# Kernel optimization log

Hardware: AMD Instinct MI355X
Metric: run time of the kernel (lower is better)

The kernel has to match this reference:

```python
import jax, jax.numpy as jnp
import numpy as np

N_NODES = 100000
N_FEAT = 500
N_HID = 16
N_CLS = 7
N_EDGES = 3200000


def setup_inputs() -> dict:
    key = jax.random.key(0)
    k1, k2, k3, k4 = jax.random.split(key, 4)
    x = jax.random.normal(k1, (N_NODES, N_FEAT), dtype=jnp.float32)
    edge_index = jax.random.randint(k2, (2, N_EDGES), 0, N_NODES, dtype=jnp.int32)
    # Glorot-style init for the two GCNConv weight matrices
    W1 = jax.random.normal(k3, (N_FEAT, N_HID), dtype=jnp.float32) * (1.0 / np.sqrt(N_FEAT))
    b1 = jnp.zeros((N_HID,), dtype=jnp.float32)
    W2 = jax.random.normal(k4, (N_HID, N_CLS), dtype=jnp.float32) * (1.0 / np.sqrt(N_HID))
    b2 = jnp.zeros((N_CLS,), dtype=jnp.float32)
    return {"x": x, "edge_index": edge_index, "W1": W1, "b1": b1, "W2": W2, "b2": b2}


def _gcn_norm(edge_index, n_nodes):
    # Add self-loops, compute symmetric normalization D^-1/2 (A+I) D^-1/2
    loop = jnp.arange(n_nodes, dtype=edge_index.dtype)
    src = jnp.concatenate([edge_index[0], loop])  # [E+N]
    dst = jnp.concatenate([edge_index[1], loop])  # [E+N]
    deg = jax.ops.segment_sum(jnp.ones_like(dst, dtype=jnp.float32), dst, num_segments=n_nodes)
    dinv = jnp.where(deg > 0, jax.lax.rsqrt(deg), 0.0)
    norm = dinv[src] * dinv[dst]  # [E+N]
    return src, dst, norm


def _gcn_conv(h, W, b, src, dst, norm, n_nodes):
    m = h @ W                                   # [N, out] dense projection first (small out dim)
    agg = jax.ops.segment_sum(m[src] * norm[:, None], dst, num_segments=n_nodes)
    return agg + b


def reference(x, edge_index, W1, b1, W2, b2):
    n = x.shape[0]
    src, dst, norm = _gcn_norm(edge_index, n)
    h = jax.nn.relu(_gcn_conv(x, W1, b1, src, dst, norm, n))
    # dropout is identity in eval mode (training=False)
    logits = _gcn_conv(h, W2, b2, src, dst, norm, n)
    return jax.nn.log_softmax(logits, axis=1)
```

## Files before the change

kernel.cpp:

```cpp
#include <hip/hip_runtime.h>
#include <math.h>

#define N_NODES 100000
#define N_EDGES 3200000
#define N_FEAT  500
#define N_HID   16
#define N_CLS   7

#define BKT_SHIFT 7
#define BKT_SIZE  128
#define NBKT      782
#define NBLK_BIN  256
#define EDGES_PER_BLK 12500
#define COUNTS_LEN (NBKT * NBLK_BIN)
#define NBLK_SCANA NBKT
#define SBUF_CAP  5632

#define OFF_DINV   0
#define OFF_COUNTS 100000
#define OFF_BSUM   300192
#define OFF_ROWP   301216
#define OFF_BINNED 401220
#define OFF_SORTED 3601220
#define OFF_WP     6801220
#define OFF_M1S    6809412
#define OFF_M2S    7609412

typedef __attribute__((ext_vector_type(8))) short short8v;
typedef __attribute__((ext_vector_type(4))) float f32x4v;

__device__ inline unsigned short f2bf(float f) {
    unsigned int u = __float_as_uint(f);
    return (unsigned short)((u + 0x7FFF + ((u >> 16) & 1)) >> 16);
}
__device__ inline float bf2f(unsigned short h) {
    return __uint_as_float((unsigned int)h << 16);
}

__global__ __launch_bounds__(1024) void hist(const int* __restrict__ dst,
                                             int* __restrict__ counts) {
    __shared__ int cnt[4][NBKT];
    int t = threadIdx.x, b = blockIdx.x;
    int wq = (t >> 6) & 3;
    for (int i = t; i < 4 * NBKT; i += 1024) ((int*)cnt)[i] = 0;
    __syncthreads();
    const int4* d4 = (const int4*)(dst + b * EDGES_PER_BLK);
    for (int k = t; k < EDGES_PER_BLK / 4; k += 1024) {
        int4 d = d4[k];
        atomicAdd(&cnt[wq][d.x >> BKT_SHIFT], 1);
        atomicAdd(&cnt[wq][d.y >> BKT_SHIFT], 1);
        atomicAdd(&cnt[wq][d.z >> BKT_SHIFT], 1);
        atomicAdd(&cnt[wq][d.w >> BKT_SHIFT], 1);
    }
    __syncthreads();
    for (int i = t; i < NBKT; i += 1024)
        counts[b * NBKT + i] = cnt[0][i] + cnt[1][i] + cnt[2][i] + cnt[3][i];
}

__global__ void scanA(int* __restrict__ counts, int* __restrict__ bsum) {
    __shared__ int s[256];
    int t = threadIdx.x, k = blockIdx.x;
    int v = counts[t * NBKT + k];
    s[t] = v;
    __syncthreads();
    for (int off = 1; off < 256; off <<= 1) {
        int a = (t >= off) ? s[t - off] : 0;
        __syncthreads();
        s[t] += a;
        __syncthreads();
    }
    counts[t * NBKT + k] = s[t] - v;
    if (t == 255) bsum[k] = s[255];
}

__global__ void scanB_wpack(int* __restrict__ bsum, const float* __restrict__ W1,
                            uint4* __restrict__ wp) {
    int t = threadIdx.x;
    {
        int p = t;
        int s = p >> 6, l = p & 63;
        int col = l & 15, kb = s * 32 + (l >> 4) * 8;
        unsigned int hw[4], lw[4];
#pragma unroll
        for (int d = 0; d < 4; ++d) {
            unsigned int hpair = 0, lpair = 0;
#pragma unroll
            for (int e = 0; e < 2; ++e) {
                int k = kb + d * 2 + e;
                float w0 = (k < N_FEAT) ? W1[k * 16 + col] : 0.f;
                unsigned int u = __float_as_uint(w0);
                unsigned int uh = u & 0xFFFF0000u;
                float res = w0 - __uint_as_float(uh);
                hpair |= (uh >> 16) << (16 * e);
                lpair |= (unsigned int)f2bf(res) << (16 * e);
            }
            hw[d] = hpair; lw[d] = lpair;
        }
        wp[p] = make_uint4(hw[0], hw[1], hw[2], hw[3]);
        wp[1024 + p] = make_uint4(lw[0], lw[1], lw[2], lw[3]);
    }
    __shared__ int s[1024];
    int v = (t < NBKT) ? bsum[t] : 0;
    s[t] = v;
    __syncthreads();
    for (int off = 1; off < 1024; off <<= 1) {
        int a = (t >= off) ? s[t - off] : 0;
        __syncthreads();
        s[t] += a;
        __syncthreads();
    }
    if (t < NBKT) bsum[t] = s[t] - v;
}

__global__ __launch_bounds__(1024) void binpass(const int* __restrict__ src,
                        const int* __restrict__ dst,
                        const int* __restrict__ counts, const int* __restrict__ bsum,
                        unsigned int* __restrict__ binned) {
    __shared__ int cur[NBKT];
    int t = threadIdx.x, b = blockIdx.x;
    for (int i = t; i < NBKT; i += 1024) cur[i] = counts[b * NBKT + i] + bsum[i];
    __syncthreads();
    const int4* s4 = (const int4*)(src + b * EDGES_PER_BLK);
    const int4* d4 = (const int4*)(dst + b * EDGES_PER_BLK);
    for (int k = t; k < EDGES_PER_BLK / 4; k += 1024) {
        int4 d = d4[k];
        int4 s = s4[k];
        int pos;
        pos = atomicAdd(&cur[d.x >> BKT_SHIFT], 1);
        binned[pos] = (unsigned int)s.x | ((unsigned int)(d.x & (BKT_SIZE - 1)) << 17);
        pos = atomicAdd(&cur[d.y >> BKT_SHIFT], 1);
        binned[pos] = (unsigned int)s.y | ((unsigned int)(d.y & (BKT_SIZE - 1)) << 17);
        pos = atomicAdd(&cur[d.z >> BKT_SHIFT], 1);
        binned[pos] = (unsigned int)s.z | ((unsigned int)(d.z & (BKT_SIZE - 1)) << 17);
        pos = atomicAdd(&cur[d.w >> BKT_SHIFT], 1);
        binned[pos] = (unsigned int)s.w | ((unsigned int)(d.w & (BKT_SIZE - 1)) << 17);
    }
}

__global__ __launch_bounds__(512) void sortA(const unsigned int* __restrict__ binned,
        const int* __restrict__ bsum,
        int* __restrict__ rowptr, float* __restrict__ dinv) {
    __shared__ int cnt[BKT_SIZE];
    __shared__ int sc[BKT_SIZE];
    int t = threadIdx.x, b = blockIdx.x;
    int beg = bsum[b];
    int end = (b < NBKT - 1) ? bsum[b + 1] : N_EDGES;
    if (t < BKT_SIZE) cnt[t] = 0;
    __syncthreads();
    for (int e = beg + t; e < end; e += 512)
        atomicAdd(&cnt[(binned[e] >> 17) & (BKT_SIZE - 1)], 1);
    __syncthreads();
    int v = (t < BKT_SIZE) ? cnt[t] : 0;
    if (t < BKT_SIZE) sc[t] = v;
    __syncthreads();
    for (int off = 1; off < BKT_SIZE; off <<= 1) {
        int a = (t < BKT_SIZE && t >= off) ? sc[t - off] : 0;
        __syncthreads();
        if (t < BKT_SIZE) sc[t] += a;
        __syncthreads();
    }
    if (t < BKT_SIZE) {
        int g = b * BKT_SIZE + t;
        if (g < N_NODES) {
            rowptr[g] = beg + sc[t] - v;
            dinv[g] = rsqrtf((float)v + 1.0f);
        }
    }
    if (b == 0 && t == 0) rowptr[N_NODES] = N_EDGES;
}

#define G1_NBLK 1563

__device__ inline void split8(const float4 a, const float4 b, short8v& hi, short8v& lo) {
    float f[8] = {a.x, a.y, a.z, a.w, b.x, b.y, b.z, b.w};
#pragma unroll
    for (int i = 0; i < 8; ++i) {
        unsigned int u = __float_as_uint(f[i]);
        unsigned int uh = u & 0xFFFF0000u;
        hi[i] = (short)(u >> 16);
        lo[i] = (short)f2bf(f[i] - __uint_as_float(uh));
    }
}

__global__ __launch_bounds__(256) void gemm1(const float* __restrict__ x,
        const uint4* __restrict__ wp, const float* __restrict__ dinv,
        unsigned short* __restrict__ m1s) {
    __shared__ uint4 swp[2048];
    const int t = threadIdx.x, b = blockIdx.x;
    const int lane = t & 63, w = t >> 6;
#pragma unroll
    for (int i = 0; i < 8; ++i) swp[i * 256 + t] = wp[i * 256 + t];
    __syncthreads();

    const int r16 = lane & 15, g = lane >> 4;
    const int rowbase = b * 64 + w * 16;
    const int row = rowbase + r16;
    const int srow = (row < N_NODES) ? row : 0;
    const float* pA = x + (size_t)srow * N_FEAT + g * 8;
    const float* t0 = (g <= 2) ? pA + 480 : x;
    const float* t1 = (g <= 1) ? pA + 484 : x;

    float4 a0_0 = *(const float4*)(pA);        float4 a1_0 = *(const float4*)(pA + 4);
    float4 a0_1 = *(const float4*)(pA + 32);   float4 a1_1 = *(const float4*)(pA + 36);
    float4 a0_2 = *(const float4*)(pA + 64);   float4 a1_2 = *(const float4*)(pA + 68);
    float4 a0_3 = *(const float4*)(pA + 96);   float4 a1_3 = *(const float4*)(pA + 100);
    float4 a0_4 = *(const float4*)(pA + 128);  float4 a1_4 = *(const float4*)(pA + 132);
    float4 a0_5 = *(const float4*)(pA + 160);  float4 a1_5 = *(const float4*)(pA + 164);

    f32x4v acc = {0.f, 0.f, 0.f, 0.f};
#pragma unroll
    for (int s = 0; s < 16; ++s) {
        float4 xa, xb;
        switch (s % 6) {
            case 0: xa = a0_0; xb = a1_0; break;
            case 1: xa = a0_1; xb = a1_1; break;
            case 2: xa = a0_2; xb = a1_2; break;
            case 3: xa = a0_3; xb = a1_3; break;
            case 4: xa = a0_4; xb = a1_4; break;
            default: xa = a0_5; xb = a1_5; break;
        }
        if (s <= 9) {
            int tg = s + 6;
            const float* p = (tg == 15) ? t0 : pA + tg * 32;
            const float* q = (tg == 15) ? t1 : pA + tg * 32 + 4;
            float4 n0 = *(const float4*)p;
            float4 n1 = *(const float4*)q;
            switch (s % 6) {
                case 0: a0_0 = n0; a1_0 = n1; break;
                case 1: a0_1 = n0; a1_1 = n1; break;
                case 2: a0_2 = n0; a1_2 = n1; break;
                case 3: a0_3 = n0; a1_3 = n1; break;
                case 4: a0_4 = n0; a1_4 = n1; break;
                default: a0_5 = n0; a1_5 = n1; break;
            }
        }
        short8v ah, al;
        split8(xa, xb, ah, al);
        short8v bh = *reinterpret_cast<const short8v*>(&swp[s * 64 + lane]);
        short8v bl = *reinterpret_cast<const short8v*>(&swp[1024 + s * 64 + lane]);
        acc = __builtin_amdgcn_mfma_f32_16x16x32_bf16(ah, bh, acc, 0, 0, 0);
        acc = __builtin_amdgcn_mfma_f32_16x16x32_bf16(al, bh, acc, 0, 0, 0);
        acc = __builtin_amdgcn_mfma_f32_16x16x32_bf16(ah, bl, acc, 0, 0, 0);
    }

#pragma unroll
    for (int j = 0; j < 4; ++j) {
        int r = rowbase + g * 4 + j;
        if (r < N_NODES) m1s[(size_t)r * 16 + r16] = f2bf(acc[j] * dinv[r]);
    }
}

__global__ __launch_bounds__(512) void sortAgg1(const unsigned int* __restrict__ binned,
        const int* __restrict__ bsum,
        const int* __restrict__ rowptr, const float* __restrict__ dinv,
        const unsigned short* __restrict__ m1s, const float* __restrict__ b1,
        const float* __restrict__ W2, unsigned int* __restrict__ sorted,
        unsigned short* __restrict__ m2s) {
    __shared__ unsigned int sbuf[SBUF_CAP];
    __shared__ int cur[BKT_SIZE];
    __shared__ float acc[BKT_SIZE * 17];
    __shared__ float sW2[N_HID * N_CLS];
    __shared__ float sb1[N_HID];
    int t = threadIdx.x, b = blockIdx.x;
    if (t < N_HID * N_CLS) sW2[t] = W2[t];
    if (t < N_HID) sb1[t] = b1[t];
    int beg = bsum[b];
    int end = (b < NBKT - 1) ? bsum[b + 1] : N_EDGES;
    if (t < BKT_SIZE) {
        int g = b * BKT_SIZE + t;
        cur[t] = ((g < N_NODES) ? rowptr[g] : end) - beg;
    }
    __syncthreads();
    for (int e = beg + t; e < end; e += 512) {
        unsigned int u = binned[e];
        int pos = atomicAdd(&cur[(u >> 17) & (BKT_SIZE - 1)], 1);
        if (pos < SBUF_CAP) sbuf[pos] = u & 0x1FFFF;
    }
    __syncthreads();
    int n = end - beg;
    for (int i = t; i < n; i += 512) sorted[beg + i] = sbuf[i];
    {
        int nn = t >> 2, q = t & 3;
        int g = b * BKT_SIZE + nn;
        float a0 = 0.f, a1 = 0.f, a2 = 0.f, a3 = 0.f;
        if (g < N_NODES) {
            int lbeg = rowptr[g] - beg;
            int lend = ((g + 1 <= N_NODES) ? rowptr[g + 1] : N_EDGES) - beg;
            int p = lbeg;
            for (; p + 3 < lend; p += 4) {
                unsigned int s0 = sbuf[p], s1 = sbuf[p + 1];
                unsigned int s2 = sbuf[p + 2], s3 = sbuf[p + 3];
                uint2 w0 = *(const uint2*)&m1s[(size_t)s0 * 16 + q * 4];
                uint2 w1 = *(const uint2*)&m1s[(size_t)s1 * 16 + q * 4];
                uint2 w2 = *(const uint2*)&m1s[(size_t)s2 * 16 + q * 4];
                uint2 w3 = *(const uint2*)&m1s[(size_t)s3 * 16 + q * 4];
                a0 += __uint_as_float(w0.x << 16);
                a1 += __uint_as_float(w0.x & 0xFFFF0000u);
                a2 += __uint_as_float(w0.y << 16);
                a3 += __uint_as_float(w0.y & 0xFFFF0000u);
                a0 += __uint_as_float(w1.x << 16);
                a1 += __uint_as_float(w1.x & 0xFFFF0000u);
                a2 += __uint_as_float(w1.y << 16);
                a3 += __uint_as_float(w1.y & 0xFFFF0000u);
                a0 += __uint_as_float(w2.x << 16);
                a1 += __uint_as_float(w2.x & 0xFFFF0000u);
                a2 += __uint_as_float(w2.y << 16);
                a3 += __uint_as_float(w2.y & 0xFFFF0000u);
                a0 += __uint_as_float(w3.x << 16);
                a1 += __uint_as_float(w3.x & 0xFFFF0000u);
                a2 += __uint_as_float(w3.y << 16);
                a3 += __uint_as_float(w3.y & 0xFFFF0000u);
            }
            for (; p < lend; ++p) {
                unsigned int s0 = sbuf[p];
                uint2 w0 = *(const uint2*)&m1s[(size_t)s0 * 16 + q * 4];
                a0 += __uint_as_float(w0.x << 16);
                a1 += __uint_as_float(w0.x & 0xFFFF0000u);
                a2 += __uint_as_float(w0.y << 16);
                a3 += __uint_as_float(w0.y & 0xFFFF0000u);
            }
        }
        __syncthreads();
        float* ap = &acc[nn * 17 + q * 4];
        ap[0] = a0; ap[1] = a1; ap[2] = a2; ap[3] = a3;
    }
    __syncthreads();
    for (int idx = t; idx < BKT_SIZE * 16; idx += 512) {
        int nn = idx >> 4, jj = idx & 15;
        int gg = b * BKT_SIZE + nn;
        if (gg < N_NODES) {
            float di = dinv[gg];
            float hv = di * (acc[nn * 17 + jj] + bf2f(m1s[(size_t)gg * 16 + jj])) + sb1[jj];
            acc[nn * 17 + jj] = hv > 0.f ? hv : 0.f;
        }
    }
    __syncthreads();
    for (int idx = t; idx < BKT_SIZE * 8; idx += 512) {
        int nn = idx >> 3, cc = idx & 7;
        int gg = b * BKT_SIZE + nn;
        if (gg < N_NODES) {
            float sum = 0.f;
            if (cc < N_CLS) {
#pragma unroll
                for (int jj = 0; jj < N_HID; ++jj) sum += acc[nn * 17 + jj] * sW2[jj * 7 + cc];
                sum *= dinv[gg];
            }
            m2s[(size_t)gg * 8 + cc] = f2bf(sum);
        }
    }
}

__global__ __launch_bounds__(512) void agg2(const unsigned int* __restrict__ sorted,
        const int* __restrict__ rowptr, const float* __restrict__ dinv,
        const unsigned short* __restrict__ m2s, const float* __restrict__ b2,
        float* __restrict__ out) {
    __shared__ float acc[BKT_SIZE * 9];
    int t = threadIdx.x, b = blockIdx.x;
    int n = t >> 2, q = t & 3;
    int g = b * BKT_SIZE + n;
    float a0 = 0.f, a1 = 0.f;
    if (g < N_NODES) {
        int beg = rowptr[g], end = rowptr[g + 1];
        int p = beg;
        for (; (p & 3) && p < end; ++p) {
            unsigned int s0 = sorted[p];
            unsigned int w0 = *(const unsigned int*)&m2s[(size_t)s0 * 8 + q * 2];
            a0 += __uint_as_float(w0 << 16); a1 += __uint_as_float(w0 & 0xFFFF0000u);
        }
        for (; p + 3 < end; p += 4) {
            uint4 sv = *(const uint4*)&sorted[p];
            unsigned int w0 = *(const unsigned int*)&m2s[(size_t)sv.x * 8 + q * 2];
            unsigned int w1 = *(const unsigned int*)&m2s[(size_t)sv.y * 8 + q * 2];
            unsigned int w2 = *(const unsigned int*)&m2s[(size_t)sv.z * 8 + q * 2];
            unsigned int w3 = *(const unsigned int*)&m2s[(size_t)sv.w * 8 + q * 2];
            a0 += __uint_as_float(w0 << 16); a1 += __uint_as_float(w0 & 0xFFFF0000u);
            a0 += __uint_as_float(w1 << 16); a1 += __uint_as_float(w1 & 0xFFFF0000u);
            a0 += __uint_as_float(w2 << 16); a1 += __uint_as_float(w2 & 0xFFFF0000u);
            a0 += __uint_as_float(w3 << 16); a1 += __uint_as_float(w3 & 0xFFFF0000u);
        }
        for (; p < end; ++p) {
            unsigned int s0 = sorted[p];
            unsigned int w0 = *(const unsigned int*)&m2s[(size_t)s0 * 8 + q * 2];
            a0 += __uint_as_float(w0 << 16); a1 += __uint_as_float(w0 & 0xFFFF0000u);
        }
    }
    float* ap = &acc[n * 9 + q * 2];
    ap[0] = a0; ap[1] = a1;
    __syncthreads();
    int j = t & 7;
    for (int pass = 0; pass < 2; ++pass) {
        int nn = (t >> 3) + pass * 64;
        int gg = b * BKT_SIZE + nn;
        bool valid = (gg < N_NODES) && (j < N_CLS);
        float v = -1e30f;
        if (valid) {
            float di = dinv[gg];
            v = di * (acc[nn * 9 + j] + bf2f(m2s[(size_t)gg * 8 + j])) + b2[j];
        }
        float mx = v;
#pragma unroll
        for (int off = 1; off < 8; off <<= 1) mx = fmaxf(mx, __shfl_xor(mx, off, 8));
        float ex = valid ? expf(v - mx) : 0.f;
        float sum = ex;
#pragma unroll
        for (int off = 1; off < 8; off <<= 1) sum += __shfl_xor(sum, off, 8);
        float ls = mx + logf(sum);
        if (valid) out[(size_t)gg * 7 + j] = v - ls;
    }
}

extern "C" void kernel_launch(void* const* d_in, const int* in_sizes, int n_in,
                              void* d_out, int out_size, void* d_ws, size_t ws_size,
                              hipStream_t stream) {
    const float* x  = (const float*)d_in[0];
    const int*   ei = (const int*)d_in[1];
    const float* W1 = (const float*)d_in[2];
    const float* b1 = (const float*)d_in[3];
    const float* W2 = (const float*)d_in[4];
    const float* b2 = (const float*)d_in[5];
    float* out = (float*)d_out;
    char*  wsb = (char*)d_ws;

    const int* src = ei;
    const int* dst = ei + N_EDGES;

    float*          dinv   = (float*)wsb + OFF_DINV;
    int*            counts = (int*)wsb + OFF_COUNTS;
    int*            bsum   = (int*)wsb + OFF_BSUM;
    int*            rowptr = (int*)wsb + OFF_ROWP;
    unsigned int*   binned = (unsigned int*)wsb + OFF_BINNED;
    unsigned int*   sorted = (unsigned int*)wsb + OFF_SORTED;
    uint4*          wp     = (uint4*)((int*)wsb + OFF_WP);
    unsigned short* m1s    = (unsigned short*)(wsb + (size_t)OFF_M1S * 4);
    unsigned short* m2s    = (unsigned short*)(wsb + (size_t)OFF_M2S * 4);

    hist       <<<NBLK_BIN, 1024, 0, stream>>>(dst, counts);
    scanA      <<<NBLK_SCANA, 256, 0, stream>>>(counts, bsum);
    scanB_wpack<<<1, 1024, 0, stream>>>(bsum, W1, wp);
    binpass    <<<NBLK_BIN, 1024, 0, stream>>>(src, dst, counts, bsum, binned);
    sortA      <<<NBKT, 512, 0, stream>>>(binned, bsum, rowptr, dinv);
    gemm1      <<<G1_NBLK, 256, 0, stream>>>(x, wp, dinv, m1s);
    sortAgg1   <<<NBKT, 512, 0, stream>>>(binned, bsum, rowptr, dinv,
                                          m1s, b1, W2, sorted, m2s);
    agg2       <<<NBKT, 512, 0, stream>>>(sorted, rowptr, dinv, m2s, b2, out);
}
```

Before: 418.2 us.

## Split per-node edge gathers across two thread halves with 1024-thread blocks

Doubles block size for sortAgg1 and agg2 so each node's neighbor list is processed by 8 threads, two interleaved halves each summing every other edge. Partial sums go to separate LDS buffers and are combined in the epilogue. This raises memory-level parallelism in the latency-bound gathers. The cost is more LDS per block and the loss of the vectorized uint4 index loads in agg2.

```diff
diff --git a/kernel.cpp b/kernel.cpp
--- a/kernel.cpp
+++ b/kernel.cpp
@@ -250,7 +250,7 @@
     }
 }
 
-__global__ __launch_bounds__(512) void sortAgg1(const unsigned int* __restrict__ binned,
+__global__ __launch_bounds__(1024) void sortAgg1(const unsigned int* __restrict__ binned,
         const int* __restrict__ bsum,
         const int* __restrict__ rowptr, const float* __restrict__ dinv,
         const unsigned short* __restrict__ m1s, const float* __restrict__ b1,
@@ -258,7 +258,7 @@
         unsigned short* __restrict__ m2s) {
     __shared__ unsigned int sbuf[SBUF_CAP];
     __shared__ int cur[BKT_SIZE];
-    __shared__ float acc[BKT_SIZE * 17];
+    __shared__ float acc[2][BKT_SIZE * 17];
     __shared__ float sW2[N_HID * N_CLS];
     __shared__ float sb1[N_HID];
     int t = threadIdx.x, b = blockIdx.x;
@@ -271,25 +271,26 @@
         cur[t] = ((g < N_NODES) ? rowptr[g] : end) - beg;
     }
     __syncthreads();
-    for (int e = beg + t; e < end; e += 512) {
+    for (int e = beg + t; e < end; e += 1024) {
         unsigned int u = binned[e];
         int pos = atomicAdd(&cur[(u >> 17) & (BKT_SIZE - 1)], 1);
         if (pos < SBUF_CAP) sbuf[pos] = u & 0x1FFFF;
     }
     __syncthreads();
     int n = end - beg;
-    for (int i = t; i < n; i += 512) sorted[beg + i] = sbuf[i];
+    for (int i = t; i < n; i += 1024) sorted[beg + i] = sbuf[i];
     {
-        int nn = t >> 2, q = t & 3;
+        int nn = t >> 3, q8 = t & 7;
+        int half = q8 >> 2, q = q8 & 3;
         int g = b * BKT_SIZE + nn;
         float a0 = 0.f, a1 = 0.f, a2 = 0.f, a3 = 0.f;
         if (g < N_NODES) {
             int lbeg = rowptr[g] - beg;
-            int lend = ((g + 1 <= N_NODES) ? rowptr[g + 1] : N_EDGES) - beg;
-            int p = lbeg;
-            for (; p + 3 < lend; p += 4) {
-                unsigned int s0 = sbuf[p], s1 = sbuf[p + 1];
-                unsigned int s2 = sbuf[p + 2], s3 = sbuf[p + 3];
+            int lend = rowptr[g + 1] - beg;
+            int p = lbeg + half;
+            for (; p + 6 < lend; p += 8) {
+                unsigned int s0 = sbuf[p],     s1 = sbuf[p + 2];
+                unsigned int s2 = sbuf[p + 4], s3 = sbuf[p + 6];
                 uint2 w0 = *(const uint2*)&m1s[(size_t)s0 * 16 + q * 4];
                 uint2 w1 = *(const uint2*)&m1s[(size_t)s1 * 16 + q * 4];
                 uint2 w2 = *(const uint2*)&m1s[(size_t)s2 * 16 + q * 4];
@@ -311,7 +312,7 @@
                 a2 += __uint_as_float(w3.y << 16);
                 a3 += __uint_as_float(w3.y & 0xFFFF0000u);
             }
-            for (; p < lend; ++p) {
+            for (; p < lend; p += 2) {
                 unsigned int s0 = sbuf[p];
                 uint2 w0 = *(const uint2*)&m1s[(size_t)s0 * 16 + q * 4];
                 a0 += __uint_as_float(w0.x << 16);
@@ -320,29 +321,29 @@
                 a3 += __uint_as_float(w0.y & 0xFFFF0000u);
             }
         }
-        __syncthreads();
-        float* ap = &acc[nn * 17 + q * 4];
+        float* ap = &acc[half][nn * 17 + q * 4];
         ap[0] = a0; ap[1] = a1; ap[2] = a2; ap[3] = a3;
     }
     __syncthreads();
-    for (int idx = t; idx < BKT_SIZE * 16; idx += 512) {
+    for (int idx = t; idx < BKT_SIZE * 16; idx += 1024) {
         int nn = idx >> 4, jj = idx & 15;
         int gg = b * BKT_SIZE + nn;
         if (gg < N_NODES) {
             float di = dinv[gg];
-            float hv = di * (acc[nn * 17 + jj] + bf2f(m1s[(size_t)gg * 16 + jj])) + sb1[jj];
-            acc[nn * 17 + jj] = hv > 0.f ? hv : 0.f;
-        }
-    }
-    __syncthreads();
-    for (int idx = t; idx < BKT_SIZE * 8; idx += 512) {
+            float hv = di * (acc[0][nn * 17 + jj] + acc[1][nn * 17 + jj]
+                             + bf2f(m1s[(size_t)gg * 16 + jj])) + sb1[jj];
+            acc[0][nn * 17 + jj] = hv > 0.f ? hv : 0.f;
+        }
+    }
+    __syncthreads();
+    for (int idx = t; idx < BKT_SIZE * 8; idx += 1024) {
         int nn = idx >> 3, cc = idx & 7;
         int gg = b * BKT_SIZE + nn;
         if (gg < N_NODES) {
             float sum = 0.f;
             if (cc < N_CLS) {
 #pragma unroll
-                for (int jj = 0; jj < N_HID; ++jj) sum += acc[nn * 17 + jj] * sW2[jj * 7 + cc];
+                for (int jj = 0; jj < N_HID; ++jj) sum += acc[0][nn * 17 + jj] * sW2[jj * 7 + cc];
                 sum *= dinv[gg];
             }
             m2s[(size_t)gg * 8 + cc] = f2bf(sum);
@@ -350,63 +351,58 @@
     }
 }
 
-__global__ __launch_bounds__(512) void agg2(const unsigned int* __restrict__ sorted,
+__global__ __launch_bounds__(1024) void agg2(const unsigned int* __restrict__ sorted,
         const int* __restrict__ rowptr, const float* __restrict__ dinv,
         const unsigned short* __restrict__ m2s, const float* __restrict__ b2,
         float* __restrict__ out) {
-    __shared__ float acc[BKT_SIZE * 9];
+    __shared__ float acc[2][BKT_SIZE * 9];
     int t = threadIdx.x, b = blockIdx.x;
-    int n = t >> 2, q = t & 3;
-    int g = b * BKT_SIZE + n;
+    int nn = t >> 3, q8 = t & 7;
+    int half = q8 >> 2, q = q8 & 3;
+    int g = b * BKT_SIZE + nn;
     float a0 = 0.f, a1 = 0.f;
     if (g < N_NODES) {
         int beg = rowptr[g], end = rowptr[g + 1];
-        int p = beg;
-        for (; (p & 3) && p < end; ++p) {
-            unsigned int s0 = sorted[p];
+        int p = beg + half;
+        for (; p + 6 < end; p += 8) {
+            unsigned int s0 = sorted[p],     s1 = sorted[p + 2];
+            unsigned int s2 = sorted[p + 4], s3 = sorted[p + 6];
             unsigned int w0 = *(const unsigned int*)&m2s[(size_t)s0 * 8 + q * 2];
-            a0 += __uint_as_float(w0 << 16); a1 += __uint_as_float(w0 & 0xFFFF0000u);
-        }
-        for (; p + 3 < end; p += 4) {
-            uint4 sv = *(const uint4*)&sorted[p];
-            unsigned int w0 = *(const unsigned int*)&m2s[(size_t)sv.x * 8 + q * 2];
-            unsigned int w1 = *(const unsigned int*)&m2s[(size_t)sv.y * 8 + q * 2];
-            unsigned int w2 = *(const unsigned int*)&m2s[(size_t)sv.z * 8 + q * 2];
-            unsigned int w3 = *(const unsigned int*)&m2s[(size_t)sv.w * 8 + q * 2];
+            unsigned int w1 = *(const unsigned int*)&m2s[(size_t)s1 * 8 + q * 2];
+            unsigned int w2 = *(const unsigned int*)&m2s[(size_t)s2 * 8 + q * 2];
+            unsigned int w3 = *(const unsigned int*)&m2s[(size_t)s3 * 8 + q * 2];
             a0 += __uint_as_float(w0 << 16); a1 += __uint_as_float(w0 & 0xFFFF0000u);
             a0 += __uint_as_float(w1 << 16); a1 += __uint_as_float(w1 & 0xFFFF0000u);
             a0 += __uint_as_float(w2 << 16); a1 += __uint_as_float(w2 & 0xFFFF0000u);
             a0 += __uint_as_float(w3 << 16); a1 += __uint_as_float(w3 & 0xFFFF0000u);
         }
-        for (; p < end; ++p) {
+        for (; p < end; p += 2) {
             unsigned int s0 = sorted[p];
             unsigned int w0 = *(const unsigned int*)&m2s[(size_t)s0 * 8 + q * 2];
             a0 += __uint_as_float(w0 << 16); a1 += __uint_as_float(w0 & 0xFFFF0000u);
         }
     }
-    float* ap = &acc[n * 9 + q * 2];
+    float* ap = &acc[half][nn * 9 + q * 2];
     ap[0] = a0; ap[1] = a1;
     __syncthreads();
     int j = t & 7;
-    for (int pass = 0; pass < 2; ++pass) {
-        int nn = (t >> 3) + pass * 64;
-        int gg = b * BKT_SIZE + nn;
-        bool valid = (gg < N_NODES) && (j < N_CLS);
-        float v = -1e30f;
-        if (valid) {
-            float di = dinv[gg];
-            v = di * (acc[nn * 9 + j] + bf2f(m2s[(size_t)gg * 8 + j])) + b2[j];
-        }
-        float mx = v;
-#pragma unroll
-        for (int off = 1; off < 8; off <<= 1) mx = fmaxf(mx, __shfl_xor(mx, off, 8));
-        float ex = valid ? expf(v - mx) : 0.f;
-        float sum = ex;
-#pragma unroll
-        for (int off = 1; off < 8; off <<= 1) sum += __shfl_xor(sum, off, 8);
-        float ls = mx + logf(sum);
-        if (valid) out[(size_t)gg * 7 + j] = v - ls;
-    }
+    int gg = b * BKT_SIZE + (t >> 3);
+    bool valid = (gg < N_NODES) && (j < N_CLS);
+    float v = -1e30f;
+    if (valid) {
+        float di = dinv[gg];
+        v = di * (acc[0][(t >> 3) * 9 + j] + acc[1][(t >> 3) * 9 + j]
+                  + bf2f(m2s[(size_t)gg * 8 + j])) + b2[j];
+    }
+    float mx = v;
+#pragma unroll
+    for (int off = 1; off < 8; off <<= 1) mx = fmaxf(mx, __shfl_xor(mx, off, 8));
+    float ex = valid ? expf(v - mx) : 0.f;
+    float sum = ex;
+#pragma unroll
+    for (int off = 1; off < 8; off <<= 1) sum += __shfl_xor(sum, off, 8);
+    float ls = mx + logf(sum);
+    if (valid) out[(size_t)gg * 7 + j] = v - ls;
 }
 
 extern "C" void kernel_launch(void* const* d_in, const int* in_sizes, int n_in,
@@ -440,7 +436,7 @@
     binpass    <<<NBLK_BIN, 1024, 0, stream>>>(src, dst, counts, bsum, binned);
     sortA      <<<NBKT, 512, 0, stream>>>(binned, bsum, rowptr, dinv);
     gemm1      <<<G1_NBLK, 256, 0, stream>>>(x, wp, dinv, m1s);
-    sortAgg1   <<<NBKT, 512, 0, stream>>>(binned, bsum, rowptr, dinv,
-                                          m1s, b1, W2, sorted, m2s);
-    agg2       <<<NBKT, 512, 0, stream>>>(sorted, rowptr, dinv, m2s, b2, out);
-}
+    sortAgg1   <<<NBKT, 1024, 0, stream>>>(binned, bsum, rowptr, dinv,
+                                           m1s, b1, W2, sorted, m2s);
+    agg2       <<<NBKT, 1024, 0, stream>>>(sorted, rowptr, dinv, m2s, b2, out);
+}
```

Measured after the change: 415.7 us. Within noise of the previous version (-0.6%).
